# Kernel tuning notes

Measured on AMD Instinct MI355X. Metric: run time of the kernel, lower is better.

## Reference

```python
import jax, jax.numpy as jnp
import numpy as np

BS, NQ, NC = 8, 100, 81      # batch, queries, classes (COCO-like)
M = 160                      # total targets across batch (20 per image)
H = W = 256                  # mask resolution
P = H * W                    # pixels per mask

COST_CLASS = 1.0
COST_MASK = 1.0
COST_DICE = 1.0


def setup_inputs() -> dict:
    key = jax.random.key(0)
    k1, k2, k3, k4 = jax.random.split(key, 4)
    return {
        "pred_logits": jax.random.normal(k1, (BS, NQ, NC), dtype=jnp.float32),
        "pred_masks": jax.random.normal(k2, (BS, NQ, H, W), dtype=jnp.float32),
        "tgt_ids": jax.random.randint(k3, (M,), 0, NC),
        # binary ground-truth masks, flattened to [M, P]
        "tgt_mask": jnp.round(jax.random.uniform(k4, (M, P), dtype=jnp.float32)),
    }


def reference(pred_logits, pred_masks, tgt_ids, tgt_mask):
    bs, nq = pred_logits.shape[:2]
    N = bs * nq

    # ---- classification cost: -softmax(logits)[:, tgt_ids]  -> [N, M]
    out_prob = jax.nn.softmax(pred_logits.reshape(N, -1), axis=-1)
    cost_class = -out_prob[:, tgt_ids]

    x = pred_masks.reshape(N, -1)          # [N, P] mask logits
    t = tgt_mask                           # [M, P] binary targets
    p = x.shape[1]

    # ---- pairwise BCE-with-logits cost, mean over pixels.
    # bce(x, t) = max(x,0) - x*t + log1p(exp(-|x|)); mean_p splits into a
    # per-prediction row term minus a matmul cross term (avoids the N x M x P blowup).
    pos = jnp.maximum(x, 0.0) + jnp.log1p(jnp.exp(-jnp.abs(x)))   # [N, P]
    row = pos.sum(axis=1)                                          # [N]
    cross = x @ t.T                                                # [N, M]
    cost_mask = (row[:, None] - cross) / p

    # ---- pairwise dice cost: 1 - (2<s,t> + 1) / (sum s + sum t + 1)
    s = jax.nn.sigmoid(x)                                          # [N, P]
    numerator = 2.0 * (s @ t.T)                                    # [N, M]
    denominator = s.sum(axis=1)[:, None] + t.sum(axis=1)[None, :]  # [N, M]
    cost_dice = 1.0 - (numerator + 1.0) / (denominator + 1.0)

    C = COST_CLASS * cost_class + COST_MASK * cost_mask + COST_DICE * cost_dice
    return C.reshape(bs, nq, -1)           # [bs, nq, M] cost matrix
```

## Files before the change

### kernel.cpp

```cpp
#include <hip/hip_runtime.h>
#include <cmath>

#define NROWS 800
#define NCLS  81
#define MT    160
#define PPX   65536
#define SSPLIT 32
#define CHUNK 2048
#define BK    64
#define RPB   32
#define RB    25

#define OFF_TBF   0
#define SZ_TBF    (MT * PPX * 2)
#define OFF_CROSS (SZ_TBF)
#define OFF_SDOT  (OFF_CROSS + NROWS * MT * 4)
#define OFF_ROW   (OFF_SDOT + NROWS * MT * 4)
#define OFF_SSUM  (OFF_ROW + NROWS * 4)
#define OFF_TSUM  (OFF_SSUM + NROWS * 4)
#define OFF_PROB  (OFF_TSUM + MT * 4)
#define OFF_END   (OFF_PROB + NROWS * NCLS * 4)

typedef __attribute__((ext_vector_type(8))) short bf16x8;
typedef __attribute__((ext_vector_type(4))) float f32x4;

typedef __attribute__((address_space(3))) char lds_char;
typedef const __attribute__((address_space(1))) char glob_char;

__device__ __forceinline__ unsigned short f2bf(float f) {
    unsigned int u = __float_as_uint(f);
    unsigned int r = (u + 0x7FFFu + ((u >> 16) & 1u)) >> 16;
    return (unsigned short)r;
}

__global__ __launch_bounds__(256) void prep_kernel(const float* __restrict__ tgt_mask,
                                                   char* __restrict__ ws) {
    int g = blockIdx.x * 256 + threadIdx.x;
    int m = g >> 13;
    int kc = g & 8191;
    int k = kc << 3;
    const float4* src = (const float4*)(tgt_mask + (size_t)m * PPX + k);
    float4 a = src[0], b = src[1];
    float part = a.x + a.y + a.z + a.w + b.x + b.y + b.z + b.w;

    uint4 o;
    o.x = (unsigned)f2bf(a.x) | ((unsigned)f2bf(a.y) << 16);
    o.y = (unsigned)f2bf(a.z) | ((unsigned)f2bf(a.w) << 16);
    o.z = (unsigned)f2bf(b.x) | ((unsigned)f2bf(b.y) << 16);
    o.w = (unsigned)f2bf(b.z) | ((unsigned)f2bf(b.w) << 16);

    int group = kc >> 3;
    int c = kc & 7;
    int oc = (group << 3) | (c ^ (m & 7));
    *(uint4*)(ws + OFF_TBF + (size_t)m * (PPX * 2) + (size_t)oc * 16) = o;

    #pragma unroll
    for (int mk = 32; mk; mk >>= 1) part += __shfl_xor(part, mk);
    __shared__ float wsum[4];
    if ((threadIdx.x & 63) == 0) wsum[threadIdx.x >> 6] = part;
    __syncthreads();
    if (threadIdx.x == 0) {
        float tot = wsum[0] + wsum[1] + wsum[2] + wsum[3];
        atomicAdd((float*)(ws + OFF_TSUM) + m, tot);
    }
}

__global__ __launch_bounds__(64) void softmax_kernel(const float* __restrict__ logits,
                                                     float* __restrict__ prob) {
    int n = blockIdx.x;
    int l = threadIdx.x;
    const float* row = logits + n * NCLS;
    float v0 = row[l];
    float v1 = (l + 64 < NCLS) ? row[l + 64] : -INFINITY;
    float mx = fmaxf(v0, v1);
    #pragma unroll
    for (int mk = 32; mk; mk >>= 1) mx = fmaxf(mx, __shfl_xor(mx, mk));
    float e0 = __expf(v0 - mx);
    float e1 = (l + 64 < NCLS) ? __expf(v1 - mx) : 0.f;
    float s = e0 + e1;
    #pragma unroll
    for (int mk = 32; mk; mk >>= 1) s += __shfl_xor(s, mk);
    float inv = 1.f / s;
    prob[n * NCLS + l] = e0 * inv;
    if (l + 64 < NCLS) prob[n * NCLS + l + 64] = e1 * inv;
}

__global__ __launch_bounds__(256) void main_kernel(const float* __restrict__ pred_masks,
                                                   char* __restrict__ ws) {
    __shared__ __align__(16) unsigned short lds_t[MT * BK];
    __shared__ __align__(16) unsigned short lds_x[RPB * BK];
    __shared__ __align__(16) unsigned short lds_s[RPB * BK];

    const int tid = threadIdx.x;
    const int w = tid >> 6, l = tid & 63;
    const int rb = blockIdx.x >> 5;
    const int s = blockIdx.x & 31;
    const int k_base = s * CHUNK;

    const int srow = tid >> 3;
    const int sc8 = tid & 7;
    const int n_glob = rb * RPB + srow;
    const float* xsrc = pred_masks + (size_t)n_glob * PPX + k_base + sc8 * 8;
    char* xw = (char*)lds_x + srow * 128 + ((sc8 ^ (srow & 7)) * 16);
    char* swp = (char*)lds_s + srow * 128 + ((sc8 ^ (srow & 7)) * 16);

    const char* tbase = ws + OFF_TBF;

    const int wr = w & 1, wc = w >> 1;
    f32x4 accX[5], accS[5];
    #pragma unroll
    for (int i = 0; i < 5; ++i) { accX[i] = (f32x4)(0.f); accS[i] = (f32x4)(0.f); }
    float rs_sp = 0.f, rs_sg = 0.f;

    for (int it = 0; it < CHUNK / BK; ++it) {
        const int k0 = k_base + it * BK;

        #pragma unroll
        for (int i = 0; i < 5; ++i) {
            int rows_base = w * 40 + i * 8;
            const char* g = (const char*)tbase
                          + (size_t)(rows_base + (l >> 3)) * (PPX * 2)
                          + (size_t)k0 * 2 + (size_t)(l & 7) * 16;
            __builtin_amdgcn_global_load_lds((glob_char*)g,
                                             (lds_char*)((char*)lds_t + rows_base * 128),
                                             16, 0, 0);
        }

        const float* xp = xsrc + it * BK;
        float4 a = *(const float4*)(xp);
        float4 b = *(const float4*)(xp + 4);
        float vx[8] = {a.x, a.y, a.z, a.w, b.x, b.y, b.z, b.w};
        bf16x8 xv, sv;
        #pragma unroll
        for (int j = 0; j < 8; ++j) {
            float v = vx[j];
            float av = fabsf(v);
            float e = __expf(-av);
            float t1 = 1.f + e;
            float r = __builtin_amdgcn_rcpf(t1);
            float sg = (v >= 0.f) ? r : e * r;
            float sp = fmaxf(v, 0.f) + __logf(t1);
            rs_sp += sp;
            rs_sg += sg;
            xv[j] = (short)f2bf(v);
            sv[j] = (short)f2bf(sg);
        }
        *(bf16x8*)xw = xv;
        *(bf16x8*)swp = sv;
        __syncthreads();

        #pragma unroll
        for (int kk = 0; kk < 2; ++kk) {
            int arow = wr * 16 + (l & 15);
            int achunk = (kk * 4 + (l >> 4)) ^ (arow & 7);
            bf16x8 ax = *(bf16x8*)((char*)lds_x + arow * 128 + achunk * 16);
            bf16x8 as = *(bf16x8*)((char*)lds_s + arow * 128 + achunk * 16);
            #pragma unroll
            for (int cf = 0; cf < 5; ++cf) {
                int mrow = (wc * 5 + cf) * 16 + (l & 15);
                int bchunk = (kk * 4 + (l >> 4)) ^ (mrow & 7);
                bf16x8 bv = *(bf16x8*)((char*)lds_t + mrow * 128 + bchunk * 16);
                accX[cf] = __builtin_amdgcn_mfma_f32_16x16x32_bf16(ax, bv, accX[cf], 0, 0, 0);
                accS[cf] = __builtin_amdgcn_mfma_f32_16x16x32_bf16(as, bv, accS[cf], 0, 0, 0);
            }
        }
        __syncthreads();
    }

    rs_sp += __shfl_xor(rs_sp, 1); rs_sp += __shfl_xor(rs_sp, 2); rs_sp += __shfl_xor(rs_sp, 4);
    rs_sg += __shfl_xor(rs_sg, 1); rs_sg += __shfl_xor(rs_sg, 2); rs_sg += __shfl_xor(rs_sg, 4);
    float* acc_row = (float*)(ws + OFF_ROW);
    float* acc_ssum = (float*)(ws + OFF_SSUM);
    if ((tid & 7) == 0) {
        atomicAdd(acc_row + n_glob, rs_sp);
        atomicAdd(acc_ssum + n_glob, rs_sg);
    }

    float* acc_cross = (float*)(ws + OFF_CROSS);
    float* acc_sdot = (float*)(ws + OFF_SDOT);
    #pragma unroll
    for (int cf = 0; cf < 5; ++cf) {
        int mcol = (wc * 5 + cf) * 16 + (l & 15);
        #pragma unroll
        for (int i = 0; i < 4; ++i) {
            int nrow = rb * RPB + wr * 16 + (l >> 4) * 4 + i;
            atomicAdd(acc_cross + nrow * MT + mcol, accX[cf][i]);
            atomicAdd(acc_sdot + nrow * MT + mcol, accS[cf][i]);
        }
    }
}

__global__ __launch_bounds__(256) void final_kernel(const int* __restrict__ tgt_ids,
                                                    const char* __restrict__ ws,
                                                    float* __restrict__ out) {
    int idx = blockIdx.x * 256 + threadIdx.x;
    int n = idx / MT;
    int m = idx - n * MT;
    const float* prob = (const float*)(ws + OFF_PROB);
    const float* acc_cross = (const float*)(ws + OFF_CROSS);
    const float* acc_sdot = (const float*)(ws + OFF_SDOT);
    const float* acc_row = (const float*)(ws + OFF_ROW);
    const float* acc_ssum = (const float*)(ws + OFF_SSUM);
    const float* tsum = (const float*)(ws + OFF_TSUM);

    float cls = -prob[n * NCLS + tgt_ids[m]];
    float cmask = (acc_row[n] - acc_cross[idx]) * (1.f / PPX);
    float cdice = 1.f - (2.f * acc_sdot[idx] + 1.f) / (acc_ssum[n] + tsum[m] + 1.f);
    out[idx] = cls + cmask + cdice;
}

extern "C" void kernel_launch(void* const* d_in, const int* in_sizes, int n_in,
                              void* d_out, int out_size, void* d_ws, size_t ws_size,
                              hipStream_t stream) {
    const float* pred_logits = (const float*)d_in[0];
    const float* pred_masks  = (const float*)d_in[1];
    const int*   tgt_ids     = (const int*)d_in[2];
    const float* tgt_mask    = (const float*)d_in[3];
    char* ws = (char*)d_ws;

    hipMemsetAsync(ws + OFF_CROSS, 0, OFF_END - OFF_CROSS, stream);
    prep_kernel<<<5120, 256, 0, stream>>>(tgt_mask, ws);
    softmax_kernel<<<NROWS, 64, 0, stream>>>(pred_logits, (float*)(ws + OFF_PROB));
    main_kernel<<<RB * SSPLIT, 256, 0, stream>>>(pred_masks, ws);
    final_kernel<<<500, 256, 0, stream>>>(tgt_ids, ws, (float*)d_out);
}
```

Before: 140.4 us.

## Drop LDS staging and feed MFMA operands directly from global memory

The main kernel no longer stages target and prediction tiles through shared memory with barriers. Each wave now loads its MFMA fragments for targets (bf16) and predictions (fp32) straight from global memory into registers, and double-buffers the prediction loads across iterations. The elementwise softplus and sigmoid work is duplicated across the two column waves, with only one wave counting each half toward the row sums. This removes LDS traffic and __syncthreads, but each wave now refetches target data that waves previously shared, which raises global and L2 traffic.

```diff
diff --git a/kernel.cpp b/kernel.cpp
--- a/kernel.cpp
+++ b/kernel.cpp
@@ -8,6 +8,7 @@
 #define SSPLIT 32
 #define CHUNK 2048
 #define BK    64
+#define ITERS (CHUNK / BK)
 #define RPB   32
 #define RB    25
 
@@ -24,9 +25,6 @@
 typedef __attribute__((ext_vector_type(8))) short bf16x8;
 typedef __attribute__((ext_vector_type(4))) float f32x4;
 
-typedef __attribute__((address_space(3))) char lds_char;
-typedef const __attribute__((address_space(1))) char glob_char;
-
 __device__ __forceinline__ unsigned short f2bf(float f) {
     unsigned int u = __float_as_uint(f);
     unsigned int r = (u + 0x7FFFu + ((u >> 16) & 1u)) >> 16;
@@ -38,8 +36,7 @@
     int g = blockIdx.x * 256 + threadIdx.x;
     int m = g >> 13;
     int kc = g & 8191;
-    int k = kc << 3;
-    const float4* src = (const float4*)(tgt_mask + (size_t)m * PPX + k);
+    const float4* src = (const float4*)(tgt_mask + (size_t)m * PPX + (kc << 3));
     float4 a = src[0], b = src[1];
     float part = a.x + a.y + a.z + a.w + b.x + b.y + b.z + b.w;
 
@@ -48,11 +45,7 @@
     o.y = (unsigned)f2bf(a.z) | ((unsigned)f2bf(a.w) << 16);
     o.z = (unsigned)f2bf(b.x) | ((unsigned)f2bf(b.y) << 16);
     o.w = (unsigned)f2bf(b.z) | ((unsigned)f2bf(b.w) << 16);
-
-    int group = kc >> 3;
-    int c = kc & 7;
-    int oc = (group << 3) | (c ^ (m & 7));
-    *(uint4*)(ws + OFF_TBF + (size_t)m * (PPX * 2) + (size_t)oc * 16) = o;
+    *(uint4*)(ws + OFF_TBF + (size_t)m * (PPX * 2) + (size_t)kc * 16) = o;
 
     #pragma unroll
     for (int mk = 32; mk; mk >>= 1) part += __shfl_xor(part, mk);
@@ -85,105 +78,136 @@
     if (l + 64 < NCLS) prob[n * NCLS + l + 64] = e1 * inv;
 }
 
+struct XS { float4 a0, a1, b0, b1; };
+
+__device__ __forceinline__ void loadx(XS& x, const float* xrow, int it) {
+    const float* p = xrow + it * BK;
+    x.a0 = *(const float4*)(p);
+    x.a1 = *(const float4*)(p + 4);
+    x.b0 = *(const float4*)(p + 32);
+    x.b1 = *(const float4*)(p + 36);
+}
+
+__device__ __forceinline__ void ew8(const float4& u, const float4& v,
+                                    bf16x8& xv, bf16x8& sv,
+                                    float& sp_acc, float& sg_acc, bool count) {
+    float vals[8] = {u.x, u.y, u.z, u.w, v.x, v.y, v.z, v.w};
+    #pragma unroll
+    for (int j = 0; j < 8; ++j) {
+        float t = vals[j];
+        float av = fabsf(t);
+        float e = __expf(-av);
+        float t1 = 1.f + e;
+        float r = __builtin_amdgcn_rcpf(t1);
+        float sg = (t >= 0.f) ? r : e * r;
+        if (count) {
+            sg_acc += sg;
+            sp_acc += fmaxf(t, 0.f) + __logf(t1);
+        }
+        xv[j] = (short)f2bf(t);
+        sv[j] = (short)f2bf(sg);
+    }
+}
+
 __global__ __launch_bounds__(256) void main_kernel(const float* __restrict__ pred_masks,
                                                    char* __restrict__ ws) {
-    __shared__ __align__(16) unsigned short lds_t[MT * BK];
-    __shared__ __align__(16) unsigned short lds_x[RPB * BK];
-    __shared__ __align__(16) unsigned short lds_s[RPB * BK];
-
     const int tid = threadIdx.x;
     const int w = tid >> 6, l = tid & 63;
     const int rb = blockIdx.x >> 5;
     const int s = blockIdx.x & 31;
     const int k_base = s * CHUNK;
 
-    const int srow = tid >> 3;
-    const int sc8 = tid & 7;
-    const int n_glob = rb * RPB + srow;
-    const float* xsrc = pred_masks + (size_t)n_glob * PPX + k_base + sc8 * 8;
-    char* xw = (char*)lds_x + srow * 128 + ((sc8 ^ (srow & 7)) * 16);
-    char* swp = (char*)lds_s + srow * 128 + ((sc8 ^ (srow & 7)) * 16);
-
-    const char* tbase = ws + OFF_TBF;
-
     const int wr = w & 1, wc = w >> 1;
+    const int lrow = l & 15;
+    const int lk = l >> 4;
+
+    const float* xrow = pred_masks + (size_t)(rb * RPB + wr * 16 + lrow) * PPX
+                      + k_base + lk * 8;
+    const unsigned short* tb = (const unsigned short*)(ws + OFF_TBF);
+    const unsigned short* tptr[5];
+    #pragma unroll
+    for (int cf = 0; cf < 5; ++cf)
+        tptr[cf] = tb + (size_t)(wc * 80 + cf * 16 + lrow) * PPX + k_base + lk * 8;
+
     f32x4 accX[5], accS[5];
     #pragma unroll
     for (int i = 0; i < 5; ++i) { accX[i] = (f32x4)(0.f); accS[i] = (f32x4)(0.f); }
     float rs_sp = 0.f, rs_sg = 0.f;
-
-    for (int it = 0; it < CHUNK / BK; ++it) {
-        const int k0 = k_base + it * BK;
-
-        #pragma unroll
-        for (int i = 0; i < 5; ++i) {
-            int rows_base = w * 40 + i * 8;
-            const char* g = (const char*)tbase
-                          + (size_t)(rows_base + (l >> 3)) * (PPX * 2)
-                          + (size_t)k0 * 2 + (size_t)(l & 7) * 16;
-            __builtin_amdgcn_global_load_lds((glob_char*)g,
-                                             (lds_char*)((char*)lds_t + rows_base * 128),
-                                             16, 0, 0);
-        }
-
-        const float* xp = xsrc + it * BK;
-        float4 a = *(const float4*)(xp);
-        float4 b = *(const float4*)(xp + 4);
-        float vx[8] = {a.x, a.y, a.z, a.w, b.x, b.y, b.z, b.w};
-        bf16x8 xv, sv;
-        #pragma unroll
-        for (int j = 0; j < 8; ++j) {
-            float v = vx[j];
-            float av = fabsf(v);
-            float e = __expf(-av);
-            float t1 = 1.f + e;
-            float r = __builtin_amdgcn_rcpf(t1);
-            float sg = (v >= 0.f) ? r : e * r;
-            float sp = fmaxf(v, 0.f) + __logf(t1);
-            rs_sp += sp;
-            rs_sg += sg;
-            xv[j] = (short)f2bf(v);
-            sv[j] = (short)f2bf(sg);
-        }
-        *(bf16x8*)xw = xv;
-        *(bf16x8*)swp = sv;
-        __syncthreads();
-
-        #pragma unroll
-        for (int kk = 0; kk < 2; ++kk) {
-            int arow = wr * 16 + (l & 15);
-            int achunk = (kk * 4 + (l >> 4)) ^ (arow & 7);
-            bf16x8 ax = *(bf16x8*)((char*)lds_x + arow * 128 + achunk * 16);
-            bf16x8 as = *(bf16x8*)((char*)lds_s + arow * 128 + achunk * 16);
+    const bool cnt0 = (wc == 0), cnt1 = (wc == 1);
+
+    XS XA, XB;
+    loadx(XA, xrow, 0);
+    loadx(XB, xrow, 1);
+
+    #pragma unroll 1
+    for (int it = 0; it < ITERS; it += 2) {
+        {
+            bf16x8 bt[2][5];
+            #pragma unroll
+            for (int kk = 0; kk < 2; ++kk)
+                #pragma unroll
+                for (int cf = 0; cf < 5; ++cf)
+                    bt[kk][cf] = *(const bf16x8*)(tptr[cf] + it * BK + kk * 32);
+
+            bf16x8 ax0, as0, ax1, as1;
+            ew8(XA.a0, XA.a1, ax0, as0, rs_sp, rs_sg, cnt0);
+            ew8(XA.b0, XA.b1, ax1, as1, rs_sp, rs_sg, cnt1);
+
+            int itn = it + 2;
+            loadx(XA, xrow, itn < ITERS ? itn : ITERS - 1);
+
             #pragma unroll
             for (int cf = 0; cf < 5; ++cf) {
-                int mrow = (wc * 5 + cf) * 16 + (l & 15);
-                int bchunk = (kk * 4 + (l >> 4)) ^ (mrow & 7);
-                bf16x8 bv = *(bf16x8*)((char*)lds_t + mrow * 128 + bchunk * 16);
-                accX[cf] = __builtin_amdgcn_mfma_f32_16x16x32_bf16(ax, bv, accX[cf], 0, 0, 0);
-                accS[cf] = __builtin_amdgcn_mfma_f32_16x16x32_bf16(as, bv, accS[cf], 0, 0, 0);
+                accX[cf] = __builtin_amdgcn_mfma_f32_16x16x32_bf16(ax0, bt[0][cf], accX[cf], 0, 0, 0);
+                accS[cf] = __builtin_amdgcn_mfma_f32_16x16x32_bf16(as0, bt[0][cf], accS[cf], 0, 0, 0);
+                accX[cf] = __builtin_amdgcn_mfma_f32_16x16x32_bf16(ax1, bt[1][cf], accX[cf], 0, 0, 0);
+                accS[cf] = __builtin_amdgcn_mfma_f32_16x16x32_bf16(as1, bt[1][cf], accS[cf], 0, 0, 0);
             }
         }
-        __syncthreads();
-    }
-
-    rs_sp += __shfl_xor(rs_sp, 1); rs_sp += __shfl_xor(rs_sp, 2); rs_sp += __shfl_xor(rs_sp, 4);
-    rs_sg += __shfl_xor(rs_sg, 1); rs_sg += __shfl_xor(rs_sg, 2); rs_sg += __shfl_xor(rs_sg, 4);
+        {
+            int itc = it + 1;
+            bf16x8 bt[2][5];
+            #pragma unroll
+            for (int kk = 0; kk < 2; ++kk)
+                #pragma unroll
+                for (int cf = 0; cf < 5; ++cf)
+                    bt[kk][cf] = *(const bf16x8*)(tptr[cf] + itc * BK + kk * 32);
+
+            bf16x8 ax0, as0, ax1, as1;
+            ew8(XB.a0, XB.a1, ax0, as0, rs_sp, rs_sg, cnt0);
+            ew8(XB.b0, XB.b1, ax1, as1, rs_sp, rs_sg, cnt1);
+
+            int itn = itc + 2;
+            loadx(XB, xrow, itn < ITERS ? itn : ITERS - 1);
+
+            #pragma unroll
+            for (int cf = 0; cf < 5; ++cf) {
+                accX[cf] = __builtin_amdgcn_mfma_f32_16x16x32_bf16(ax0, bt[0][cf], accX[cf], 0, 0, 0);
+                accS[cf] = __builtin_amdgcn_mfma_f32_16x16x32_bf16(as0, bt[0][cf], accS[cf], 0, 0, 0);
+                accX[cf] = __builtin_amdgcn_mfma_f32_16x16x32_bf16(ax1, bt[1][cf], accX[cf], 0, 0, 0);
+                accS[cf] = __builtin_amdgcn_mfma_f32_16x16x32_bf16(as1, bt[1][cf], accS[cf], 0, 0, 0);
+            }
+        }
+    }
+
+    rs_sp += __shfl_xor(rs_sp, 16); rs_sp += __shfl_xor(rs_sp, 32);
+    rs_sg += __shfl_xor(rs_sg, 16); rs_sg += __shfl_xor(rs_sg, 32);
     float* acc_row = (float*)(ws + OFF_ROW);
     float* acc_ssum = (float*)(ws + OFF_SSUM);
-    if ((tid & 7) == 0) {
-        atomicAdd(acc_row + n_glob, rs_sp);
-        atomicAdd(acc_ssum + n_glob, rs_sg);
+    if (l < 16) {
+        int n = rb * RPB + wr * 16 + l;
+        atomicAdd(acc_row + n, rs_sp);
+        atomicAdd(acc_ssum + n, rs_sg);
     }
 
     float* acc_cross = (float*)(ws + OFF_CROSS);
     float* acc_sdot = (float*)(ws + OFF_SDOT);
     #pragma unroll
     for (int cf = 0; cf < 5; ++cf) {
-        int mcol = (wc * 5 + cf) * 16 + (l & 15);
+        int mcol = wc * 80 + cf * 16 + lrow;
         #pragma unroll
         for (int i = 0; i < 4; ++i) {
-            int nrow = rb * RPB + wr * 16 + (l >> 4) * 4 + i;
+            int nrow = rb * RPB + wr * 16 + lk * 4 + i;
             atomicAdd(acc_cross + nrow * MT + mcol, accX[cf][i]);
             atomicAdd(acc_sdot + nrow * MT + mcol, accS[cf][i]);
         }
```

Result: slower. 332.5 us (+136.9%).

## Double-buffer target tiles and prefetch mask logits in main GEMM loop

Applied to the files above, without the earlier changes.

The main kernel gets a double-buffered LDS tile for the bf16 targets, with the next tile's async global-to-LDS load issued before the current tile's compute. Mask logits are register-prefetched two iterations ahead, and waits use explicit vmcnt/lgkmcnt counts. The elementwise math also changes: softplus is computed as log(1+exp(x)) through exp2/log2 hardware intrinsics with a clamp, and sigmoid becomes t/(1+t), which cuts instructions per element. This adds LDS use, relies on a hand-counted vmcnt(9), and may lose softplus accuracy for large negative inputs.

```diff
diff --git a/kernel.cpp b/kernel.cpp
--- a/kernel.cpp
+++ b/kernel.cpp
@@ -8,6 +8,7 @@
 #define SSPLIT 32
 #define CHUNK 2048
 #define BK    64
+#define ITERS (CHUNK / BK)
 #define RPB   32
 #define RB    25
 
@@ -38,8 +39,7 @@
     int g = blockIdx.x * 256 + threadIdx.x;
     int m = g >> 13;
     int kc = g & 8191;
-    int k = kc << 3;
-    const float4* src = (const float4*)(tgt_mask + (size_t)m * PPX + k);
+    const float4* src = (const float4*)(tgt_mask + (size_t)m * PPX + (kc << 3));
     float4 a = src[0], b = src[1];
     float part = a.x + a.y + a.z + a.w + b.x + b.y + b.z + b.w;
 
@@ -85,9 +85,35 @@
     if (l + 64 < NCLS) prob[n * NCLS + l + 64] = e1 * inv;
 }
 
+struct XS { float4 a; float4 b; };
+
+__device__ __forceinline__ void loadx(XS& x, const float* xrow, int it) {
+    const float* p = xrow + it * BK;
+    x.a = *(const float4*)(p);
+    x.b = *(const float4*)(p + 4);
+}
+
+__device__ __forceinline__ void ew8(const XS& xs, bf16x8& xv, bf16x8& sv,
+                                    float& slog2, float& sg_acc) {
+    float vals[8] = {xs.a.x, xs.a.y, xs.a.z, xs.a.w, xs.b.x, xs.b.y, xs.b.z, xs.b.w};
+    #pragma unroll
+    for (int j = 0; j < 8; ++j) {
+        float v = vals[j];
+        float vl = fminf(v * 1.44269504089f, 126.f);
+        float t2 = __builtin_amdgcn_exp2f(vl);
+        float d = 1.f + t2;
+        float r = __builtin_amdgcn_rcpf(d);
+        float sg = t2 * r;
+        slog2 += __builtin_amdgcn_logf(d);
+        sg_acc += sg;
+        xv[j] = (short)f2bf(v);
+        sv[j] = (short)f2bf(sg);
+    }
+}
+
 __global__ __launch_bounds__(256) void main_kernel(const float* __restrict__ pred_masks,
                                                    char* __restrict__ ws) {
-    __shared__ __align__(16) unsigned short lds_t[MT * BK];
+    __shared__ __align__(16) unsigned short lds_t[2][MT * BK];
     __shared__ __align__(16) unsigned short lds_x[RPB * BK];
     __shared__ __align__(16) unsigned short lds_s[RPB * BK];
 
@@ -100,21 +126,14 @@
     const int srow = tid >> 3;
     const int sc8 = tid & 7;
     const int n_glob = rb * RPB + srow;
-    const float* xsrc = pred_masks + (size_t)n_glob * PPX + k_base + sc8 * 8;
+    const float* xrow = pred_masks + (size_t)n_glob * PPX + k_base + sc8 * 8;
     char* xw = (char*)lds_x + srow * 128 + ((sc8 ^ (srow & 7)) * 16);
     char* swp = (char*)lds_s + srow * 128 + ((sc8 ^ (srow & 7)) * 16);
 
     const char* tbase = ws + OFF_TBF;
 
-    const int wr = w & 1, wc = w >> 1;
-    f32x4 accX[5], accS[5];
-    #pragma unroll
-    for (int i = 0; i < 5; ++i) { accX[i] = (f32x4)(0.f); accS[i] = (f32x4)(0.f); }
-    float rs_sp = 0.f, rs_sg = 0.f;
-
-    for (int it = 0; it < CHUNK / BK; ++it) {
-        const int k0 = k_base + it * BK;
-
+    auto stage_t = [&](int b, int tt) {
+        const int k0 = k_base + tt * BK;
         #pragma unroll
         for (int i = 0; i < 5; ++i) {
             int rows_base = w * 40 + i * 8;
@@ -122,51 +141,74 @@
                           + (size_t)(rows_base + (l >> 3)) * (PPX * 2)
                           + (size_t)k0 * 2 + (size_t)(l & 7) * 16;
             __builtin_amdgcn_global_load_lds((glob_char*)g,
-                                             (lds_char*)((char*)lds_t + rows_base * 128),
+                                             (lds_char*)((char*)lds_t[b] + rows_base * 128),
                                              16, 0, 0);
         }
-
-        const float* xp = xsrc + it * BK;
-        float4 a = *(const float4*)(xp);
-        float4 b = *(const float4*)(xp + 4);
-        float vx[8] = {a.x, a.y, a.z, a.w, b.x, b.y, b.z, b.w};
-        bf16x8 xv, sv;
+    };
+
+    const int wr = w & 1, wc = w >> 1;
+    f32x4 accX[5], accS[5];
+    #pragma unroll
+    for (int i = 0; i < 5; ++i) { accX[i] = (f32x4)(0.f); accS[i] = (f32x4)(0.f); }
+    float slog2 = 0.f, rs_sg = 0.f;
+
+    stage_t(0, 0);
+    XS XA, XB;
+    loadx(XA, xrow, 0);
+    loadx(XB, xrow, 1);
+
+    #pragma unroll 1
+    for (int it = 0; it < ITERS; it += 2) {
         #pragma unroll
-        for (int j = 0; j < 8; ++j) {
-            float v = vx[j];
-            float av = fabsf(v);
-            float e = __expf(-av);
-            float t1 = 1.f + e;
-            float r = __builtin_amdgcn_rcpf(t1);
-            float sg = (v >= 0.f) ? r : e * r;
-            float sp = fmaxf(v, 0.f) + __logf(t1);
-            rs_sp += sp;
-            rs_sg += sg;
-            xv[j] = (short)f2bf(v);
-            sv[j] = (short)f2bf(sg);
+        for (int half = 0; half < 2; ++half) {
+            const int h = it + half;
+            const int hb = half;
+
+            int tn = h + 1; if (tn >= ITERS) tn = ITERS - 1;
+            stage_t(hb ^ 1, tn);
+            __builtin_amdgcn_sched_barrier(0);
+
+            bf16x8 xv, sv;
+            if (half == 0) ew8(XA, xv, sv, slog2, rs_sg);
+            else           ew8(XB, xv, sv, slog2, rs_sg);
+            *(bf16x8*)xw = xv;
+            *(bf16x8*)swp = sv;
+
+            int tr = h + 2; if (tr >= ITERS) tr = ITERS - 1;
+            if (half == 0) loadx(XA, xrow, tr);
+            else           loadx(XB, xrow, tr);
+
+            asm volatile("s_waitcnt vmcnt(9) lgkmcnt(0)" ::: "memory");
+            __builtin_amdgcn_sched_barrier(0);
+            __builtin_amdgcn_s_barrier();
+            __builtin_amdgcn_sched_barrier(0);
+
+            #pragma unroll
+            for (int kk = 0; kk < 2; ++kk) {
+                int arow = wr * 16 + (l & 15);
+                int achunk = (kk * 4 + (l >> 4)) ^ (arow & 7);
+                bf16x8 ax = *(bf16x8*)((char*)lds_x + arow * 128 + achunk * 16);
+                bf16x8 as = *(bf16x8*)((char*)lds_s + arow * 128 + achunk * 16);
+                #pragma unroll
+                for (int cf = 0; cf < 5; ++cf) {
+                    int mrow = (wc * 5 + cf) * 16 + (l & 15);
+                    int bchunk = (kk * 4 + (l >> 4)) ^ (mrow & 7);
+                    bf16x8 bv = *(bf16x8*)((char*)lds_t[hb] + mrow * 128 + bchunk * 16);
+                    accX[cf] = __builtin_amdgcn_mfma_f32_16x16x32_bf16(ax, bv, accX[cf], 0, 0, 0);
+                    accS[cf] = __builtin_amdgcn_mfma_f32_16x16x32_bf16(as, bv, accS[cf], 0, 0, 0);
+                }
+            }
+
+            asm volatile("s_waitcnt lgkmcnt(0)" ::: "memory");
+            __builtin_amdgcn_sched_barrier(0);
+            __builtin_amdgcn_s_barrier();
+            __builtin_amdgcn_sched_barrier(0);
         }
-        *(bf16x8*)xw = xv;
-        *(bf16x8*)swp = sv;
-        __syncthreads();
-
-        #pragma unroll
-        for (int kk = 0; kk < 2; ++kk) {
-            int arow = wr * 16 + (l & 15);
-            int achunk = (kk * 4 + (l >> 4)) ^ (arow & 7);
-            bf16x8 ax = *(bf16x8*)((char*)lds_x + arow * 128 + achunk * 16);
-            bf16x8 as = *(bf16x8*)((char*)lds_s + arow * 128 + achunk * 16);
-            #pragma unroll
-            for (int cf = 0; cf < 5; ++cf) {
-                int mrow = (wc * 5 + cf) * 16 + (l & 15);
-                int bchunk = (kk * 4 + (l >> 4)) ^ (mrow & 7);
-                bf16x8 bv = *(bf16x8*)((char*)lds_t + mrow * 128 + bchunk * 16);
-                accX[cf] = __builtin_amdgcn_mfma_f32_16x16x32_bf16(ax, bv, accX[cf], 0, 0, 0);
-                accS[cf] = __builtin_amdgcn_mfma_f32_16x16x32_bf16(as, bv, accS[cf], 0, 0, 0);
-            }
-        }
-        __syncthreads();
-    }
-
+    }
+
+    asm volatile("s_waitcnt vmcnt(0)" ::: "memory");
+
+    float rs_sp = slog2 * 0.69314718056f;
     rs_sp += __shfl_xor(rs_sp, 1); rs_sp += __shfl_xor(rs_sp, 2); rs_sp += __shfl_xor(rs_sp, 4);
     rs_sg += __shfl_xor(rs_sg, 1); rs_sg += __shfl_xor(rs_sg, 2); rs_sg += __shfl_xor(rs_sg, 4);
     float* acc_row = (float*)(ws + OFF_ROW);
@@ -218,7 +260,7 @@
     const float* tgt_mask    = (const float*)d_in[3];
     char* ws = (char*)d_ws;
 
-    hipMemsetAsync(ws + OFF_CROSS, 0, OFF_END - OFF_CROSS, stream);
+    (void)hipMemsetAsync(ws + OFF_CROSS, 0, OFF_END - OFF_CROSS, stream);
     prep_kernel<<<5120, 256, 0, stream>>>(tgt_mask, ws);
     softmax_kernel<<<NROWS, 64, 0, stream>>>(pred_logits, (float*)(ws + OFF_PROB));
     main_kernel<<<RB * SSPLIT, 256, 0, stream>>>(pred_masks, ws);
```

After: 137.4 us. 1.02x faster.
